# Kernel tuning notes

Hardware: AMD Instinct MI355X
Metric: run time of the kernel (lower is better)

The kernel has to match this reference:

```python
import jax, jax.numpy as jnp
import numpy as np

N = 100000
E = 1600000
D_IN = 128
D_OUT = 128
D_DEC = 2
TAU = 0.5
NEG_SLOPE = 0.2  # PyG GATv2Conv default negative_slope


def _glorot(key, shape):
    lim = (6.0 / (shape[0] + shape[1])) ** 0.5
    return jax.random.uniform(key, shape, jnp.float32, -lim, lim)


def gatv2(x, edge_index, Wl, Wr, bl, br, att, bias):
    """PyG GATv2Conv, heads=1, add_self_loops=True, eval mode (no dropout).
    out[i] = sum_j softmax_i( att . leaky_relu(xl[j] + xr[i]) ) * xl[j] + bias
    """
    n = x.shape[0]
    loops = jnp.arange(n, dtype=edge_index.dtype)
    src = jnp.concatenate([edge_index[0], loops])  # [E+N]
    dst = jnp.concatenate([edge_index[1], loops])
    xl = x @ Wl + bl  # [N, out]
    xr = x @ Wr + br
    # per-edge unnormalized score
    e = jax.nn.leaky_relu(xl[src] + xr[dst], NEG_SLOPE) @ att  # [E+N]
    # scatter-softmax over incoming edges of each target node
    m = jax.ops.segment_max(e, dst, num_segments=n)
    a = jnp.exp(e - m[dst])
    s = jax.ops.segment_sum(a, dst, num_segments=n)
    alpha = a / (s[dst] + 1e-16)
    out = jax.ops.segment_sum(alpha[:, None] * xl[src], dst, num_segments=n)
    return out + bias


def setup_inputs() -> dict:
    key = jax.random.key(0)
    ks = jax.random.split(key, 16)
    x = jax.random.normal(ks[0], (N, D_IN), jnp.float32)
    edge_dec = jax.random.randint(ks[1], (2, E), 0, N, jnp.int64)
    edge_0 = jax.random.randint(ks[2], (2, E), 0, N, jnp.int64)
    edge_1 = jax.random.randint(ks[3], (2, E), 0, N, jnp.int64)
    u = jax.random.uniform(ks[4], (N, D_DEC), jnp.float32, 1e-6, 1.0 - 1e-6)
    gumbel = -jnp.log(-jnp.log(u))  # Gumbel(0,1) noise
    # shared GAT (used for every decision branch)
    Wl_g = _glorot(ks[5], (D_IN, D_OUT))
    Wr_g = _glorot(ks[6], (D_IN, D_OUT))
    bl_g = jnp.zeros((D_OUT,), jnp.float32)
    br_g = jnp.zeros((D_OUT,), jnp.float32)
    att_g = _glorot(ks[7], (D_OUT, 1))[:, 0]
    bias_g = jnp.zeros((D_OUT,), jnp.float32)
    # decision GAT
    Wl_d = _glorot(ks[8], (D_IN, D_DEC))
    Wr_d = _glorot(ks[9], (D_IN, D_DEC))
    bl_d = jnp.zeros((D_DEC,), jnp.float32)
    br_d = jnp.zeros((D_DEC,), jnp.float32)
    att_d = _glorot(ks[10], (D_DEC, 1))[:, 0]
    bias_d = jnp.zeros((D_DEC,), jnp.float32)
    return {"x": x, "edge_dec": edge_dec, "edge_0": edge_0, "edge_1": edge_1,
            "gumbel": gumbel,
            "Wl_g": Wl_g, "Wr_g": Wr_g, "bl_g": bl_g, "br_g": br_g,
            "att_g": att_g, "bias_g": bias_g,
            "Wl_d": Wl_d, "Wr_d": Wr_d, "bl_d": bl_d, "br_d": br_d,
            "att_d": att_d, "bias_d": bias_d}


def reference(x, edge_dec, edge_0, edge_1, gumbel,
              Wl_g, Wr_g, bl_g, br_g, att_g, bias_g,
              Wl_d, Wr_d, bl_d, br_d, att_d, bias_d):
    # decision logits via decision GAT on the decision edge set
    logits = gatv2(x, edge_dec, Wl_d, Wr_d, bl_d, br_d, att_d, bias_d)  # [N, 2]
    # hard gumbel-softmax with straight-through estimator, tau=0.5
    y_soft = jax.nn.softmax((logits + gumbel) / TAU, axis=-1)
    idx = jnp.argmax(y_soft, axis=-1)
    y_hard = jax.nn.one_hot(idx, y_soft.shape[-1], dtype=y_soft.dtype)
    decisions = y_hard + y_soft - jax.lax.stop_gradient(y_soft)
    # per-decision GAT (shared weights, different edge sets), gated sum
    out = jnp.zeros((x.shape[0], Wl_g.shape[1]), x.dtype)
    for i, ei in enumerate([edge_0, edge_1]):
        out = out + gatv2(x, ei, Wl_g, Wr_g, bl_g, br_g, att_g, bias_g) * decisions[:, i:i + 1]
    return out
```

## Files before the change

kernel.cpp:

```cpp
#include <hip/hip_runtime.h>

#define NEG 0.2f
#define CAPD16 384
#define CAPC16 704
#define CH 9216
#define NT 512
#define CSH 9
#define FPC 32
#define NCMAX 256
#define CHB 512
#define CCAPD 9216
#define CCAPC 17408

typedef __attribute__((ext_vector_type(8))) short short8;
typedef __attribute__((ext_vector_type(4))) float f32x4;

static __device__ __forceinline__ unsigned short f2bf(float f) {
  unsigned u = __float_as_uint(f);
  u += 0x7fffu + ((u >> 16) & 1u);
  return (unsigned short)(u >> 16);
}
static __device__ __forceinline__ float bflo(unsigned u) {
  return __uint_as_float(u << 16);
}
static __device__ __forceinline__ float bfhi(unsigned u) {
  return __uint_as_float(u & 0xffff0000u);
}
static __device__ __forceinline__ float bfx(const uint4& v, int f) {
  unsigned c = (f < 2) ? v.x : (f < 4) ? v.y : (f < 6) ? v.z : v.w;
  return (f & 1) ? bfhi(c) : bflo(c);
}
static __device__ __forceinline__ unsigned f2u(float f) {
  unsigned b = __float_as_uint(f);
  return (b & 0x80000000u) ? ~b : (b | 0x80000000u);
}
static __device__ __forceinline__ float u2f(unsigned u) {
  unsigned b = (u & 0x80000000u) ? (u ^ 0x80000000u) : ~u;
  return __uint_as_float(b);
}

__global__ void k_prep_wt(const float* __restrict__ Wl, const float* __restrict__ Wr,
                          unsigned short* __restrict__ wt, int* __restrict__ gccur,
                          int ncur) {
  if (blockIdx.x < 128) {
    int idx = blockIdx.x * 256 + threadIdx.x;
    int c = idx >> 7, k = idx & 127;
    float v = (c < 128) ? Wl[(size_t)k * 128 + c] : Wr[(size_t)k * 128 + (c - 128)];
    wt[idx] = f2bf(v);
  } else {
    int i = (blockIdx.x - 128) * 256 + threadIdx.x;
    if (i < ncur) gccur[i] = 0;
  }
}

__global__ __launch_bounds__(256) void k_gemm_main(
    const float* __restrict__ x, const unsigned short* __restrict__ wt,
    const float* __restrict__ bl, const float* __restrict__ br,
    const float* __restrict__ Wld, const float* __restrict__ Wrd,
    const float* __restrict__ bld, const float* __restrict__ brd,
    unsigned short* __restrict__ xl, unsigned short* __restrict__ xr,
    float* __restrict__ xld, float* __restrict__ xrd, int N) {
  __shared__ unsigned short sx[32][272];
  int w = threadIdx.x >> 6, lane = threadIdx.x & 63;
  int m = lane & 15, quad = lane >> 4;
  int rowbase = blockIdx.x * 32;
  if (rowbase >= N) return;
  int colbase = w * 64;
  f32x4 acc0[4] = {}, acc1[4] = {};
  float dl0 = 0.f, dl1 = 0.f, dr0 = 0.f, dr1 = 0.f;
  int rc0 = rowbase + m;      if (rc0 >= N) rc0 = N - 1;
  int rc1 = rowbase + 16 + m; if (rc1 >= N) rc1 = N - 1;
  const float* arow0 = x + (size_t)rc0 * 128 + quad * 8;
  const float* arow1 = x + (size_t)rc1 * 128 + quad * 8;
#pragma unroll
  for (int kb = 0; kb < 128; kb += 32) {
    float4 a00 = *(const float4*)(arow0 + kb);
    float4 a01 = *(const float4*)(arow0 + kb + 4);
    float4 a10 = *(const float4*)(arow1 + kb);
    float4 a11 = *(const float4*)(arow1 + kb + 4);
    if (w < 2) {
      float4 A = (w == 0) ? a00 : a10;
      float4 B = (w == 0) ? a01 : a11;
      int k0 = kb + quad * 8;
      const float4* wl4 = (const float4*)(Wld + 2 * k0);
      const float4* wr4 = (const float4*)(Wrd + 2 * k0);
      float4 l0 = wl4[0], l1 = wl4[1], l2 = wl4[2], l3 = wl4[3];
      float4 r0 = wr4[0], r1 = wr4[1], r2 = wr4[2], r3 = wr4[3];
      dl0 = fmaf(A.x, l0.x, dl0); dl1 = fmaf(A.x, l0.y, dl1);
      dl0 = fmaf(A.y, l0.z, dl0); dl1 = fmaf(A.y, l0.w, dl1);
      dl0 = fmaf(A.z, l1.x, dl0); dl1 = fmaf(A.z, l1.y, dl1);
      dl0 = fmaf(A.w, l1.z, dl0); dl1 = fmaf(A.w, l1.w, dl1);
      dl0 = fmaf(B.x, l2.x, dl0); dl1 = fmaf(B.x, l2.y, dl1);
      dl0 = fmaf(B.y, l2.z, dl0); dl1 = fmaf(B.y, l2.w, dl1);
      dl0 = fmaf(B.z, l3.x, dl0); dl1 = fmaf(B.z, l3.y, dl1);
      dl0 = fmaf(B.w, l3.z, dl0); dl1 = fmaf(B.w, l3.w, dl1);
      dr0 = fmaf(A.x, r0.x, dr0); dr1 = fmaf(A.x, r0.y, dr1);
      dr0 = fmaf(A.y, r0.z, dr0); dr1 = fmaf(A.y, r0.w, dr1);
      dr0 = fmaf(A.z, r1.x, dr0); dr1 = fmaf(A.z, r1.y, dr1);
      dr0 = fmaf(A.w, r1.z, dr0); dr1 = fmaf(A.w, r1.w, dr1);
      dr0 = fmaf(B.x, r2.x, dr0); dr1 = fmaf(B.x, r2.y, dr1);
      dr0 = fmaf(B.y, r2.z, dr0); dr1 = fmaf(B.y, r2.w, dr1);
      dr0 = fmaf(B.z, r3.x, dr0); dr1 = fmaf(B.z, r3.y, dr1);
      dr0 = fmaf(B.w, r3.z, dr0); dr1 = fmaf(B.w, r3.w, dr1);
    }
    short8 af0, af1;
    af0[0] = (short)f2bf(a00.x); af0[1] = (short)f2bf(a00.y);
    af0[2] = (short)f2bf(a00.z); af0[3] = (short)f2bf(a00.w);
    af0[4] = (short)f2bf(a01.x); af0[5] = (short)f2bf(a01.y);
    af0[6] = (short)f2bf(a01.z); af0[7] = (short)f2bf(a01.w);
    af1[0] = (short)f2bf(a10.x); af1[1] = (short)f2bf(a10.y);
    af1[2] = (short)f2bf(a10.z); af1[3] = (short)f2bf(a10.w);
    af1[4] = (short)f2bf(a11.x); af1[5] = (short)f2bf(a11.y);
    af1[6] = (short)f2bf(a11.z); af1[7] = (short)f2bf(a11.w);
#pragma unroll
    for (int ct = 0; ct < 4; ct++) {
      const unsigned short* bp =
          wt + (size_t)(colbase + ct * 16 + m) * 128 + kb + quad * 8;
      short8 bfr = *(const short8*)bp;
      acc0[ct] = __builtin_amdgcn_mfma_f32_16x16x32_bf16(af0, bfr, acc0[ct], 0, 0, 0);
      acc1[ct] = __builtin_amdgcn_mfma_f32_16x16x32_bf16(af1, bfr, acc1[ct], 0, 0, 0);
    }
  }
  if (w < 2) {
    dl0 += __shfl_xor(dl0, 16); dl0 += __shfl_xor(dl0, 32);
    dl1 += __shfl_xor(dl1, 16); dl1 += __shfl_xor(dl1, 32);
    dr0 += __shfl_xor(dr0, 16); dr0 += __shfl_xor(dr0, 32);
    dr1 += __shfl_xor(dr1, 16); dr1 += __shfl_xor(dr1, 32);
    if (quad == 0) {
      int row = rowbase + w * 16 + m;
      if (row < N) {
        float2 vl; vl.x = dl0 + bld[0]; vl.y = dl1 + bld[1];
        float2 vr; vr.x = dr0 + brd[0]; vr.y = dr1 + brd[1];
        *(float2*)(xld + 2 * (size_t)row) = vl;
        *(float2*)(xrd + 2 * (size_t)row) = vr;
      }
    }
  }
#pragma unroll
  for (int ct = 0; ct < 4; ct++) {
    int c = colbase + ct * 16 + m;
    float badd = (c < 128) ? bl[c] : br[c - 128];
#pragma unroll
    for (int r = 0; r < 4; r++) {
      sx[quad * 4 + r][c]      = f2bf(acc0[ct][r] + badd);
      sx[16 + quad * 4 + r][c] = f2bf(acc1[ct][r] + badd);
    }
  }
  __syncthreads();
  {
    int row = threadIdx.x >> 3, chunk = threadIdx.x & 7;
    int gr = rowbase + row;
    if (gr < N) {
      const uint4* src = (const uint4*)&sx[row][chunk * 32];
      uint4* dst = (chunk < 4)
          ? (uint4*)(xl + (size_t)gr * 128 + chunk * 32)
          : (uint4*)(xr + (size_t)gr * 128 + (chunk - 4) * 32);
      dst[0] = src[0]; dst[1] = src[1]; dst[2] = src[2]; dst[3] = src[3];
    }
  }
}

__global__ __launch_bounds__(NT) void k_bin_coarse(
    const int* __restrict__ ed, const int* __restrict__ e0,
    const int* __restrict__ e1, int* __restrict__ gccur,
    unsigned* __restrict__ cbind, unsigned* __restrict__ cbinc,
    long E, int NC) {
  __shared__ unsigned stage[CH];
  __shared__ int h[CHB + 1];
  __shared__ int gbase[CHB];
  __shared__ int wtot[8], wexcl[8];
  int tid = threadIdx.x;
  long base = (long)blockIdx.x * CH;
  long T = 3 * E;
  for (int a = tid; a < CHB + 1; a += NT) h[a] = 0;
  __syncthreads();
  unsigned pays[CH / NT];
  int has[CH / NT];
#pragma unroll
  for (int it = 0; it < CH / NT; it++) {
    long idx = base + it * NT + tid;
    int ha = -1; unsigned pay = 0;
    if (idx < T) {
      if (idx < E) {
        int s = ed[idx], t = ed[E + idx];
        ha = t >> CSH;
        pay = ((unsigned)s << CSH) | (unsigned)(t & ((1 << CSH) - 1));
      } else {
        int k = idx >= 2 * E;
        const int* L = k ? e1 : e0;
        long j = idx - E - (k ? E : 0);
        int s = L[j], t = L[E + j];
        ha = NCMAX + (t >> CSH);
        pay = ((unsigned)s << (CSH + 1)) | ((unsigned)k << CSH) |
              (unsigned)(t & ((1 << CSH) - 1));
      }
      atomicAdd(&h[ha], 1);
    }
    pays[it] = pay; has[it] = ha;
  }
  __syncthreads();
  {
    int v = h[tid];
    int lane = tid & 63, wv = tid >> 6;
    int inc = v;
    for (int off = 1; off < 64; off <<= 1) {
      int nv = __shfl_up(inc, off);
      if (lane >= off) inc += nv;
    }
    if (lane == 63) wtot[wv] = inc;
    __syncthreads();
    if (tid == 0) {
      int r = 0;
      for (int i = 0; i < 8; i++) { wexcl[i] = r; r += wtot[i]; }
    }
    __syncthreads();
    int excl = wexcl[wv] + inc - v;
    h[tid] = excl;
    if (tid == NT - 1) h[CHB] = excl + v;
  }
  __syncthreads();
  {
    int a = tid;
    int cnt = h[a + 1] - h[a];
    if (cnt > 0) {
      if (a < NCMAX) { if (a < NC) gbase[a] = atomicAdd(&gccur[a], cnt); }
      else { int b = a - NCMAX; if (b < NC) gbase[a] = atomicAdd(&gccur[NC + b], cnt); }
    }
  }
  __syncthreads();
#pragma unroll
  for (int it = 0; it < CH / NT; it++) {
    int ha = has[it];
    if (ha >= 0) {
      int pos = atomicAdd(&h[ha], 1);
      stage[pos] = pays[it];
    }
  }
  __syncthreads();
  int lane = tid & 63, wv = tid >> 6;
  for (int a = wv; a < 2 * NCMAX; a += 8) {
    int start = a ? h[a - 1] : 0;
    int end = h[a];
    int len = end - start;
    if (len <= 0) continue;
    int gb = gbase[a];
    if (a < NCMAX) {
      if (a < NC) {
        unsigned* dst = cbind + (size_t)a * CCAPD;
        for (int i = lane; i < len; i += 64) {
          int o = gb + i;
          if (o < CCAPD) dst[o] = stage[start + i];
        }
      }
    } else {
      int b = a - NCMAX;
      if (b < NC) {
        unsigned* dst = cbinc + (size_t)b * CCAPC;
        for (int i = lane; i < len; i += 64) {
          int o = gb + i;
          if (o < CCAPC) dst[o] = stage[start + i];
        }
      }
    }
  }
}

__global__ __launch_bounds__(NT) void k_bin_fine(
    const unsigned* __restrict__ cbind, const unsigned* __restrict__ cbinc,
    const int* __restrict__ gccur, unsigned* __restrict__ bind,
    unsigned* __restrict__ binc, int* __restrict__ cntd, int* __restrict__ cntc,
    int NC, int NB16) {
  __shared__ int cur[FPC];
  int cb = blockIdx.x;
  int isC = cb >= NC;
  int c = isC ? cb - NC : cb;
  int cnt = gccur[cb];
  int ccap = isC ? CCAPC : CCAPD;
  if (cnt > ccap) cnt = ccap;
  const unsigned* src = isC ? (cbinc + (size_t)c * CCAPC)
                            : (cbind + (size_t)c * CCAPD);
  int tid = threadIdx.x;
  if (tid < FPC) cur[tid] = 0;
  __syncthreads();
  if (isC) {
    for (int i = tid; i < cnt; i += NT) {
      unsigned pay = src[i];
      int f = (pay >> 4) & (FPC - 1);
      int fb = c * FPC + f;
      int pos = atomicAdd(&cur[f], 1);
      unsigned o = ((pay >> (CSH + 1)) << 5) | (((pay >> CSH) & 1u) << 4) |
                   (pay & 15u);
      if (pos < CAPC16 && fb < NB16) binc[(size_t)fb * CAPC16 + pos] = o;
    }
  } else {
    for (int i = tid; i < cnt; i += NT) {
      unsigned pay = src[i];
      int f = (pay >> 4) & (FPC - 1);
      int fb = c * FPC + f;
      int pos = atomicAdd(&cur[f], 1);
      unsigned o = ((pay >> CSH) << 4) | (pay & 15u);
      if (pos < CAPD16 && fb < NB16) bind[(size_t)fb * CAPD16 + pos] = o;
    }
  }
  __syncthreads();
  if (tid < FPC) {
    int fb = c * FPC + tid;
    if (fb < NB16) {
      if (isC) { int v = cur[tid]; if (v > CAPC16) v = CAPC16; cntc[fb] = v; }
      else     { int v = cur[tid]; if (v > CAPD16) v = CAPD16; cntd[fb] = v; }
    }
  }
}

__global__ __launch_bounds__(256) void k_fused(
    const unsigned* __restrict__ bind, const unsigned* __restrict__ binc,
    const int* __restrict__ cntd_, const int* __restrict__ cntc_,
    const unsigned short* __restrict__ xl, const unsigned short* __restrict__ xr,
    const float* __restrict__ xld, const float* __restrict__ xrd,
    const float* __restrict__ attd, const float* __restrict__ biasd,
    const float* __restrict__ g, const float* __restrict__ att,
    const float* __restrict__ bias, float* __restrict__ out, int N) {
  __shared__ float xrd_s[32];
  __shared__ unsigned nmax[16];
  __shared__ float nsum[16], na0[16], na1[16];
  __shared__ int dec_s[16], scnt[16];
  __shared__ int slots[16 * 65];
  int tid = threadIdx.x;
  int b = blockIdx.x, nb0 = b << 4;
  int cdn = cntd_[b]; if (cdn > CAPD16) cdn = CAPD16;
  int ccn = cntc_[b]; if (ccn > CAPC16) ccn = CAPC16;
  float a0 = attd[0], a1 = attd[1];
  float eself = 0.f, x0s = 0.f, x1s = 0.f;
  if (tid < 16) {
    int node = nb0 + tid;
    if (node < N) {
      float2 xrv = *(const float2*)(xrd + 2 * (size_t)node);
      xrd_s[2 * tid] = xrv.x; xrd_s[2 * tid + 1] = xrv.y;
      float2 xlv = *(const float2*)(xld + 2 * (size_t)node);
      x0s = xlv.x; x1s = xlv.y;
      float h0 = x0s + xrv.x, h1 = x1s + xrv.y;
      eself = a0 * fmaxf(h0, NEG * h0) + a1 * fmaxf(h1, NEG * h1);
      nmax[tid] = f2u(eself);
    } else {
      xrd_s[2 * tid] = 0.f; xrd_s[2 * tid + 1] = 0.f;
      nmax[tid] = f2u(0.f);
    }
    nsum[tid] = 0.f; na0[tid] = 0.f; na1[tid] = 0.f;
  }
  __syncthreads();
  const unsigned* bd = bind + (size_t)b * CAPD16;
  const float2* xld2 = (const float2*)xld;
  auto dscore = [&](float2 v, int tl) {
    float h0 = v.x + xrd_s[2 * tl], h1 = v.y + xrd_s[2 * tl + 1];
    return a0 * fmaxf(h0, NEG * h0) + a1 * fmaxf(h1, NEG * h1);
  };
  unsigned pkA = 0, pkB = 0;
  float2 vA, vB; vA.x = vA.y = vB.x = vB.y = 0.f;
  float sA = 0.f, sB = 0.f;
  bool okA = tid < cdn, okB = tid + 256 < cdn;
  if (okA) {
    pkA = bd[tid]; vA = xld2[pkA >> 4];
    sA = dscore(vA, pkA & 15);
    atomicMax(&nmax[pkA & 15], f2u(sA));
  }
  if (okB) {
    pkB = bd[tid + 256]; vB = xld2[pkB >> 4];
    sB = dscore(vB, pkB & 15);
    atomicMax(&nmax[pkB & 15], f2u(sB));
  }
  __syncthreads();
  if (okA) {
    int tl = pkA & 15;
    float w = expf(sA - u2f(nmax[tl]));
    atomicAdd(&nsum[tl], w); atomicAdd(&na0[tl], w * vA.x); atomicAdd(&na1[tl], w * vA.y);
  }
  if (okB) {
    int tl = pkB & 15;
    float w = expf(sB - u2f(nmax[tl]));
    atomicAdd(&nsum[tl], w); atomicAdd(&na0[tl], w * vB.x); atomicAdd(&na1[tl], w * vB.y);
  }
  __syncthreads();
  if (tid < 16) {
    int node = nb0 + tid;
    if (node < N) {
      float mm = u2f(nmax[tid]);
      float ws = expf(eself - mm);
      float den = nsum[tid] + ws + 1e-16f;
      float z0 = (na0[tid] + ws * x0s) / den + biasd[0] + g[2 * (size_t)node];
      float z1 = (na1[tid] + ws * x1s) / den + biasd[1] + g[2 * (size_t)node + 1];
      dec_s[tid] = (z1 > z0) ? 1 : 0;
      scnt[tid] = 1; slots[tid * 65] = node;
    } else {
      dec_s[tid] = -1; scnt[tid] = 0; slots[tid * 65] = 0;
    }
  }
  __syncthreads();
  const unsigned* bc = binc + (size_t)b * CAPC16;
  for (int i = tid; i < ccn; i += 256) {
    unsigned pk = bc[i];
    int tl = pk & 15, k = (pk >> 4) & 1;
    if (k == dec_s[tl]) {
      int pos = atomicAdd(&scnt[tl], 1);
      if (pos < 64) slots[tl * 65 + pos] = pk >> 5;
    }
  }
  __syncthreads();

  int l = tid & 15, gg = tid >> 4;
  const float4* at4 = (const float4*)att;
  float4 atA = at4[l * 2], atB = at4[l * 2 + 1];
  float a6[8] = {0.6f * atA.x, 0.6f * atA.y, 0.6f * atA.z, 0.6f * atA.w,
                 0.6f * atB.x, 0.6f * atB.y, 0.6f * atB.z, 0.6f * atB.w};
  float a4[8] = {0.4f * atA.x, 0.4f * atA.y, 0.4f * atA.z, 0.4f * atA.w,
                 0.4f * atB.x, 0.4f * atB.y, 0.4f * atB.z, 0.4f * atB.w};
  const float4* b4 = (const float4*)bias;
  float4 bA = b4[l * 2], bB = b4[l * 2 + 1];

  int nd = nb0 + gg;
  bool nvalid = nd < N;
  int cnt = scnt[gg]; if (cnt > 64) cnt = 64;
  if (!nvalid) cnt = 0;
  int mc = max(cnt, __shfl_xor(cnt, 16));
  mc = max(mc, __shfl_xor(mc, 32));

  int nc = nvalid ? nd : 0;
  uint4 xrp = ((const uint4*)(xr + (size_t)nc * 128))[l];
  float xrv[8] = {bflo(xrp.x), bfhi(xrp.x), bflo(xrp.y), bfhi(xrp.y),
                  bflo(xrp.z), bfhi(xrp.z), bflo(xrp.w), bfhi(xrp.w)};

  int cl = cnt - 1; if (cl < 0) cl = 0;
  const int* srow = &slots[gg * 65];
  uint4 cur[4];
#pragma unroll
  for (int j = 0; j < 4; j++) {
    int idx = j > cl ? cl : j;
    cur[j] = ((const uint4*)(xl + (size_t)srow[idx] * 128))[l];
  }
  float m = -3.0e38f, lsum = 0.f;
  float gacc[8] = {0.f, 0.f, 0.f, 0.f, 0.f, 0.f, 0.f, 0.f};

  for (int e = 0; e < mc; e += 4) {
    uint4 nxt[4];
#pragma unroll
    for (int j = 0; j < 4; j++) {
      int idx = e + 4 + j; if (idx > cl) idx = cl;
      nxt[j] = ((const uint4*)(xl + (size_t)srow[idx] * 128))[l];
    }
    float p[4];
#pragma unroll
    for (int j = 0; j < 4; j++) {
      float pa = 0.f, pb = 0.f;
#pragma unroll
      for (int f = 0; f < 8; f++) {
        float h = bfx(cur[j], f) + xrv[f];
        pa = fmaf(a6[f], h, pa);
        pb = fmaf(a4[f], fabsf(h), pb);
      }
      p[j] = pa + pb;
    }
#pragma unroll
    for (int off = 1; off < 16; off <<= 1) {
      p[0] += __shfl_xor(p[0], off); p[1] += __shfl_xor(p[1], off);
      p[2] += __shfl_xor(p[2], off); p[3] += __shfl_xor(p[3], off);
    }
    float pe0 = (e     < cnt) ? p[0] : -3.0e38f;
    float pe1 = (e + 1 < cnt) ? p[1] : -3.0e38f;
    float pe2 = (e + 2 < cnt) ? p[2] : -3.0e38f;
    float pe3 = (e + 3 < cnt) ? p[3] : -3.0e38f;
    float nm = fmaxf(m, fmaxf(fmaxf(pe0, pe1), fmaxf(pe2, pe3)));
    float sc = __expf(m - nm);
    float w0 = __expf(pe0 - nm), w1 = __expf(pe1 - nm);
    float w2 = __expf(pe2 - nm), w3 = __expf(pe3 - nm);
    lsum = lsum * sc + w0 + w1 + w2 + w3;
#pragma unroll
    for (int f = 0; f < 8; f++) {
      float t0 = fmaf(w0, bfx(cur[0], f), gacc[f] * sc);
      float t1 = fmaf(w1, bfx(cur[1], f), t0);
      float t2 = fmaf(w2, bfx(cur[2], f), t1);
      gacc[f]  = fmaf(w3, bfx(cur[3], f), t2);
    }
    m = nm;
#pragma unroll
    for (int j = 0; j < 4; j++) cur[j] = nxt[j];
  }
  if (nvalid) {
    float inv = 1.0f / (lsum + 1e-16f);
    float4 oA, oB;
    oA.x = gacc[0] * inv + bA.x; oA.y = gacc[1] * inv + bA.y;
    oA.z = gacc[2] * inv + bA.z; oA.w = gacc[3] * inv + bA.w;
    oB.x = gacc[4] * inv + bB.x; oB.y = gacc[5] * inv + bB.y;
    oB.z = gacc[6] * inv + bB.z; oB.w = gacc[7] * inv + bB.w;
    float4* op = (float4*)(out + (size_t)nd * 128 + l * 8);
    op[0] = oA; op[1] = oB;
  }
}

extern "C" void kernel_launch(void* const* d_in, const int* in_sizes, int n_in,
                              void* d_out, int out_size, void* d_ws, size_t ws_size,
                              hipStream_t stream) {
  const float* x      = (const float*)d_in[0];
  const int*   ed     = (const int*)d_in[1];
  const int*   e0     = (const int*)d_in[2];
  const int*   e1     = (const int*)d_in[3];
  const float* gumbel = (const float*)d_in[4];
  const float* Wl_g   = (const float*)d_in[5];
  const float* Wr_g   = (const float*)d_in[6];
  const float* bl_g   = (const float*)d_in[7];
  const float* br_g   = (const float*)d_in[8];
  const float* att_g  = (const float*)d_in[9];
  const float* bias_g = (const float*)d_in[10];
  const float* Wl_d   = (const float*)d_in[11];
  const float* Wr_d   = (const float*)d_in[12];
  const float* bl_d   = (const float*)d_in[13];
  const float* br_d   = (const float*)d_in[14];
  const float* att_d  = (const float*)d_in[15];
  const float* bias_d = (const float*)d_in[16];

  const int  N    = in_sizes[0] / 128;
  const long E    = in_sizes[1] / 2;
  const int  NB16 = (N + 15) / 16;
  const int  NC   = (N + (1 << CSH) - 1) >> CSH;

  char* p = (char*)d_ws;
  auto alloc = [&](size_t bytes) -> void* {
    void* r = (void*)p;
    p += (bytes + 255) & ~(size_t)255;
    return r;
  };
  unsigned short* xl = (unsigned short*)alloc((size_t)N * 128 * 2);
  unsigned short* xr = (unsigned short*)alloc((size_t)N * 128 * 2);
  unsigned short* wt = (unsigned short*)alloc((size_t)256 * 128 * 2);
  float* xld      = (float*)alloc((size_t)N * 2 * 4);
  float* xrd      = (float*)alloc((size_t)N * 2 * 4);
  int* gccur      = (int*)alloc((size_t)2 * NC * 4);
  int* cntd       = (int*)alloc((size_t)NB16 * 4);
  int* cntc       = (int*)alloc((size_t)NB16 * 4);
  unsigned* bind  = (unsigned*)alloc((size_t)NB16 * CAPD16 * 4);
  unsigned* binc  = (unsigned*)alloc((size_t)NB16 * CAPC16 * 4);
  unsigned* cbind = (unsigned*)xl;
  unsigned* cbinc = (unsigned*)xr;

  const int gB = (int)((3 * E + CH - 1) / CH);
  const int gZ = (2 * NC + 255) / 256;

  k_prep_wt<<<128 + gZ, 256, 0, stream>>>(Wl_g, Wr_g, wt, gccur, 2 * NC);
  k_bin_coarse<<<gB, NT, 0, stream>>>(ed, e0, e1, gccur, cbind, cbinc, E, NC);
  k_bin_fine<<<2 * NC, NT, 0, stream>>>(cbind, cbinc, gccur, bind, binc,
                                        cntd, cntc, NC, NB16);
  k_gemm_main<<<(N + 31) / 32, 256, 0, stream>>>(x, wt, bl_g, br_g, Wl_d, Wr_d,
                                                 bl_d, br_d, xl, xr, xld, xrd, N);
  k_fused<<<NB16, 256, 0, stream>>>(bind, binc, cntd, cntc, xl, xr, xld, xrd,
                                    att_d, bias_d, gumbel, att_g, bias_g,
                                    (float*)d_out, N);
}
```

Measured before the change: 367.8 us.

## Split fine binning across slices with global atomics; widen fused edge loop to 8

The fine binning kernel now launches four blocks per coarse bin instead of one. Each block builds a shared-memory histogram of its slice, reserves output ranges through global atomics on the per-bin counters, and scatters payloads held in registers. The zeroing of those counters moves into the prep kernel. The fused attention kernel processes and prefetches 8 neighbour rows per iteration instead of 4, exposing more memory-level parallelism at the cost of more registers. Per-bin counters are no longer clamped to capacity, and the output order within a bin is no longer deterministic.

```diff
diff --git a/kernel.cpp b/kernel.cpp
--- a/kernel.cpp
+++ b/kernel.cpp
@@ -7,10 +7,12 @@
 #define NT 512
 #define CSH 9
 #define FPC 32
+#define NSL 4
 #define NCMAX 256
 #define CHB 512
 #define CCAPD 9216
 #define CCAPC 17408
+#define FIT 9
 
 typedef __attribute__((ext_vector_type(8))) short short8;
 typedef __attribute__((ext_vector_type(4))) float f32x4;
@@ -40,7 +42,7 @@
 }
 
 __global__ void k_prep_wt(const float* __restrict__ Wl, const float* __restrict__ Wr,
-                          unsigned short* __restrict__ wt, int* __restrict__ gccur,
+                          unsigned short* __restrict__ wt, int* __restrict__ zbuf,
                           int ncur) {
   if (blockIdx.x < 128) {
     int idx = blockIdx.x * 256 + threadIdx.x;
@@ -49,7 +51,7 @@
     wt[idx] = f2bf(v);
   } else {
     int i = (blockIdx.x - 128) * 256 + threadIdx.x;
-    if (i < ncur) gccur[i] = 0;
+    if (i < ncur) zbuf[i] = 0;
   }
 }
 
@@ -270,44 +272,61 @@
     const int* __restrict__ gccur, unsigned* __restrict__ bind,
     unsigned* __restrict__ binc, int* __restrict__ cntd, int* __restrict__ cntc,
     int NC, int NB16) {
-  __shared__ int cur[FPC];
-  int cb = blockIdx.x;
+  __shared__ int hh[FPC];
+  __shared__ int gb[FPC];
+  int blk = blockIdx.x;
+  int cb = blk >> 2, sl = blk & (NSL - 1);
   int isC = cb >= NC;
   int c = isC ? cb - NC : cb;
   int cnt = gccur[cb];
   int ccap = isC ? CCAPC : CCAPD;
   if (cnt > ccap) cnt = ccap;
+  int ssz = (cnt + NSL - 1) / NSL;
+  int s0 = sl * ssz;
+  int s1 = s0 + ssz; if (s1 > cnt) s1 = cnt;
   const unsigned* src = isC ? (cbinc + (size_t)c * CCAPC)
                             : (cbind + (size_t)c * CCAPD);
   int tid = threadIdx.x;
-  if (tid < FPC) cur[tid] = 0;
-  __syncthreads();
-  if (isC) {
-    for (int i = tid; i < cnt; i += NT) {
-      unsigned pay = src[i];
-      int f = (pay >> 4) & (FPC - 1);
+  if (tid < FPC) hh[tid] = 0;
+  __syncthreads();
+  unsigned pays[FIT]; int fs[FIT];
+#pragma unroll
+  for (int it = 0; it < FIT; it++) {
+    int i = s0 + it * NT + tid;
+    int f = -1; unsigned pay = 0;
+    if (i < s1) {
+      pay = src[i];
+      f = (pay >> 4) & (FPC - 1);
+      atomicAdd(&hh[f], 1);
+    }
+    pays[it] = pay; fs[it] = f;
+  }
+  __syncthreads();
+  if (tid < FPC) {
+    int v = hh[tid];
+    int base = 0;
+    int fb = c * FPC + tid;
+    if (v > 0 && fb < NB16)
+      base = atomicAdd(isC ? &cntc[fb] : &cntd[fb], v);
+    gb[tid] = base;
+    hh[tid] = 0;
+  }
+  __syncthreads();
+#pragma unroll
+  for (int it = 0; it < FIT; it++) {
+    int f = fs[it];
+    if (f >= 0) {
+      unsigned pay = pays[it];
       int fb = c * FPC + f;
-      int pos = atomicAdd(&cur[f], 1);
-      unsigned o = ((pay >> (CSH + 1)) << 5) | (((pay >> CSH) & 1u) << 4) |
-                   (pay & 15u);
-      if (pos < CAPC16 && fb < NB16) binc[(size_t)fb * CAPC16 + pos] = o;
-    }
-  } else {
-    for (int i = tid; i < cnt; i += NT) {
-      unsigned pay = src[i];
-      int f = (pay >> 4) & (FPC - 1);
-      int fb = c * FPC + f;
-      int pos = atomicAdd(&cur[f], 1);
-      unsigned o = ((pay >> CSH) << 4) | (pay & 15u);
-      if (pos < CAPD16 && fb < NB16) bind[(size_t)fb * CAPD16 + pos] = o;
-    }
-  }
-  __syncthreads();
-  if (tid < FPC) {
-    int fb = c * FPC + tid;
-    if (fb < NB16) {
-      if (isC) { int v = cur[tid]; if (v > CAPC16) v = CAPC16; cntc[fb] = v; }
-      else     { int v = cur[tid]; if (v > CAPD16) v = CAPD16; cntd[fb] = v; }
+      int pos = gb[f] + atomicAdd(&hh[f], 1);
+      if (isC) {
+        unsigned o = ((pay >> (CSH + 1)) << 5) | (((pay >> CSH) & 1u) << 4) |
+                     (pay & 15u);
+        if (pos < CAPC16 && fb < NB16) binc[(size_t)fb * CAPC16 + pos] = o;
+      } else {
+        unsigned o = ((pay >> CSH) << 4) | (pay & 15u);
+        if (pos < CAPD16 && fb < NB16) bind[(size_t)fb * CAPD16 + pos] = o;
+      }
     }
   }
 }
@@ -413,8 +432,6 @@
                  0.6f * atB.x, 0.6f * atB.y, 0.6f * atB.z, 0.6f * atB.w};
   float a4[8] = {0.4f * atA.x, 0.4f * atA.y, 0.4f * atA.z, 0.4f * atA.w,
                  0.4f * atB.x, 0.4f * atB.y, 0.4f * atB.z, 0.4f * atB.w};
-  const float4* b4 = (const float4*)bias;
-  float4 bA = b4[l * 2], bB = b4[l * 2 + 1];
 
   int nd = nb0 + gg;
   bool nvalid = nd < N;
@@ -430,25 +447,25 @@
 
   int cl = cnt - 1; if (cl < 0) cl = 0;
   const int* srow = &slots[gg * 65];
-  uint4 cur[4];
-#pragma unroll
-  for (int j = 0; j < 4; j++) {
+  uint4 cur[8];
+#pragma unroll
+  for (int j = 0; j < 8; j++) {
     int idx = j > cl ? cl : j;
     cur[j] = ((const uint4*)(xl + (size_t)srow[idx] * 128))[l];
   }
   float m = -3.0e38f, lsum = 0.f;
   float gacc[8] = {0.f, 0.f, 0.f, 0.f, 0.f, 0.f, 0.f, 0.f};
 
-  for (int e = 0; e < mc; e += 4) {
-    uint4 nxt[4];
-#pragma unroll
-    for (int j = 0; j < 4; j++) {
-      int idx = e + 4 + j; if (idx > cl) idx = cl;
+  for (int e = 0; e < mc; e += 8) {
+    uint4 nxt[8];
+#pragma unroll
+    for (int j = 0; j < 8; j++) {
+      int idx = e + 8 + j; if (idx > cl) idx = cl;
       nxt[j] = ((const uint4*)(xl + (size_t)srow[idx] * 128))[l];
     }
-    float p[4];
-#pragma unroll
-    for (int j = 0; j < 4; j++) {
+    float p[8];
+#pragma unroll
+    for (int j = 0; j < 8; j++) {
       float pa = 0.f, pb = 0.f;
 #pragma unroll
       for (int f = 0; f < 8; f++) {
@@ -460,30 +477,32 @@
     }
 #pragma unroll
     for (int off = 1; off < 16; off <<= 1) {
-      p[0] += __shfl_xor(p[0], off); p[1] += __shfl_xor(p[1], off);
-      p[2] += __shfl_xor(p[2], off); p[3] += __shfl_xor(p[3], off);
-    }
-    float pe0 = (e     < cnt) ? p[0] : -3.0e38f;
-    float pe1 = (e + 1 < cnt) ? p[1] : -3.0e38f;
-    float pe2 = (e + 2 < cnt) ? p[2] : -3.0e38f;
-    float pe3 = (e + 3 < cnt) ? p[3] : -3.0e38f;
-    float nm = fmaxf(m, fmaxf(fmaxf(pe0, pe1), fmaxf(pe2, pe3)));
+#pragma unroll
+      for (int j = 0; j < 8; j++) p[j] += __shfl_xor(p[j], off);
+    }
+#pragma unroll
+    for (int j = 0; j < 8; j++) p[j] = (e + j < cnt) ? p[j] : -3.0e38f;
+    float nm = m;
+#pragma unroll
+    for (int j = 0; j < 8; j++) nm = fmaxf(nm, p[j]);
     float sc = __expf(m - nm);
-    float w0 = __expf(pe0 - nm), w1 = __expf(pe1 - nm);
-    float w2 = __expf(pe2 - nm), w3 = __expf(pe3 - nm);
-    lsum = lsum * sc + w0 + w1 + w2 + w3;
-#pragma unroll
-    for (int f = 0; f < 8; f++) {
-      float t0 = fmaf(w0, bfx(cur[0], f), gacc[f] * sc);
-      float t1 = fmaf(w1, bfx(cur[1], f), t0);
-      float t2 = fmaf(w2, bfx(cur[2], f), t1);
-      gacc[f]  = fmaf(w3, bfx(cur[3], f), t2);
+    lsum *= sc;
+#pragma unroll
+    for (int f = 0; f < 8; f++) gacc[f] *= sc;
+#pragma unroll
+    for (int j = 0; j < 8; j++) {
+      float w = __expf(p[j] - nm);
+      lsum += w;
+#pragma unroll
+      for (int f = 0; f < 8; f++) gacc[f] = fmaf(w, bfx(cur[j], f), gacc[f]);
     }
     m = nm;
 #pragma unroll
-    for (int j = 0; j < 4; j++) cur[j] = nxt[j];
+    for (int j = 0; j < 8; j++) cur[j] = nxt[j];
   }
   if (nvalid) {
+    const float4* b4 = (const float4*)bias;
+    float4 bA = b4[l * 2], bB = b4[l * 2 + 1];
     float inv = 1.0f / (lsum + 1e-16f);
     float4 oA, oB;
     oA.x = gacc[0] * inv + bA.x; oA.y = gacc[1] * inv + bA.y;
@@ -532,21 +551,23 @@
   unsigned short* wt = (unsigned short*)alloc((size_t)256 * 128 * 2);
   float* xld      = (float*)alloc((size_t)N * 2 * 4);
   float* xrd      = (float*)alloc((size_t)N * 2 * 4);
-  int* gccur      = (int*)alloc((size_t)2 * NC * 4);
-  int* cntd       = (int*)alloc((size_t)NB16 * 4);
-  int* cntc       = (int*)alloc((size_t)NB16 * 4);
+  const int nz    = 2 * NC + 2 * NB16;
+  int* zbuf       = (int*)alloc((size_t)nz * 4);
   unsigned* bind  = (unsigned*)alloc((size_t)NB16 * CAPD16 * 4);
   unsigned* binc  = (unsigned*)alloc((size_t)NB16 * CAPC16 * 4);
+  int* gccur = zbuf;
+  int* cntd  = zbuf + 2 * NC;
+  int* cntc  = cntd + NB16;
   unsigned* cbind = (unsigned*)xl;
   unsigned* cbinc = (unsigned*)xr;
 
   const int gB = (int)((3 * E + CH - 1) / CH);
-  const int gZ = (2 * NC + 255) / 256;
-
-  k_prep_wt<<<128 + gZ, 256, 0, stream>>>(Wl_g, Wr_g, wt, gccur, 2 * NC);
+  const int gZ = (nz + 255) / 256;
+
+  k_prep_wt<<<128 + gZ, 256, 0, stream>>>(Wl_g, Wr_g, wt, zbuf, nz);
   k_bin_coarse<<<gB, NT, 0, stream>>>(ed, e0, e1, gccur, cbind, cbinc, E, NC);
-  k_bin_fine<<<2 * NC, NT, 0, stream>>>(cbind, cbinc, gccur, bind, binc,
-                                        cntd, cntc, NC, NB16);
+  k_bin_fine<<<2 * NC * NSL, NT, 0, stream>>>(cbind, cbinc, gccur, bind, binc,
+                                              cntd, cntc, NC, NB16);
   k_gemm_main<<<(N + 31) / 32, 256, 0, stream>>>(x, wt, bl_g, br_g, Wl_d, Wr_d,
                                                  bl_d, br_d, xl, xr, xld, xrd, N);
   k_fused<<<NB16, 256, 0, stream>>>(bind, binc, cntd, cntc, xl, xr, xld, xrd,
```

New measurement: 382.0 us. +3.8%, slower.
